# Optimization experiments

Hardware: AMD Instinct MI355X
Metric: run time of the kernel (lower is better)

The kernel has to match this reference:

```python
import jax, jax.numpy as jnp
import numpy as np

B, C, L = 8192, 1, 4096
SCALES = 5
OUT_DIM = 512
STD_FACTOR = 1.0
SQRT_HALF = 0.7071067811865476  # Haar filter coefficient 1/sqrt(2)


def setup_inputs() -> dict:
    key = jax.random.key(0)
    k1, k2 = jax.random.split(key)
    x = jax.random.normal(k1, (B, C, L), dtype=jnp.float32)
    # kaiming_uniform_(a=0): bound = sqrt(2) * sqrt(3 / fan_in)
    fan_in = L  # in_dim_wave == in_dim for dyadic Haar
    bound = np.sqrt(2.0) * np.sqrt(3.0 / fan_in)
    block_mat = jax.random.uniform(k2, (L, OUT_DIM), dtype=jnp.float32,
                                   minval=-bound, maxval=bound)
    return {"x": x, "block_mat": block_mat}


def haar_analysis(x, scales):
    """Multi-level Haar DWT over last axis. Returns [cA_n, cD_n, ..., cD_1]."""
    details = []
    cur = x
    for _ in range(scales):
        even, odd = cur[..., ::2], cur[..., 1::2]
        details.append((even - odd) * SQRT_HALF)  # highpass
        cur = (even + odd) * SQRT_HALF            # lowpass
    return [cur] + details[::-1]


def reference(x, block_mat):
    coeffs = haar_analysis(x, SCALES)
    x_freq_cat = jnp.concatenate(coeffs, axis=-1)        # [B, C, L]
    c_no = x_freq_cat.shape[-1]
    x_freq_mat = x_freq_cat.reshape(-1, c_no)            # [B*C, L]
    a = jnp.abs(x_freq_mat)
    # torch.std is unbiased (ddof=1)
    threshold = jnp.mean(a) + jnp.std(a, ddof=1) * STD_FACTOR
    mask = a > threshold
    # sparse.mm(sparse(masked x), W) == (x * mask) @ W
    x_sparse = jnp.where(mask, x_freq_mat, jnp.zeros((), x_freq_mat.dtype))
    out = jax.nn.relu(x_sparse @ block_mat)              # [B*C, OUT_DIM]
    return out.reshape(x_freq_cat.shape[:-1] + (OUT_DIM,))
```

## Files before the change

### kernel.cpp

```cpp
#include <hip/hip_runtime.h>
#include <hip/hip_bf16.h>
#include <math.h>

#define LDIM 4096
#define NROWS 8192
#define NOUT 512

static const float SQRT_HALF_F = 0.70710678118654752440f;

typedef __attribute__((ext_vector_type(8))) short short8;
typedef __attribute__((ext_vector_type(4))) float f32x4;
typedef __attribute__((ext_vector_type(8))) unsigned short u16x8;
typedef __attribute__((ext_vector_type(4))) unsigned short u16x4;
typedef __attribute__((ext_vector_type(2))) unsigned short u16x2;

#define AM_OFF   0ull
#define WT_OFF   67108864ull
#define PART_OFF (WT_OFF + 4194304ull)
#define THR_OFF  (PART_OFF + 131072ull)

__device__ inline unsigned short f2bf(float f) {
  union { float f; unsigned u; } v; v.f = f;
  unsigned r = (v.u + 0x7fffu + ((v.u >> 16) & 1u)) >> 16;
  return (unsigned short)r;
}

__device__ inline unsigned short mcvt(float f, float thr) {
  return f2bf((fabsf(f) > thr) ? f : 0.0f);
}

__device__ inline void async16(void* l, const void* g) {
  __builtin_amdgcn_global_load_lds((const __attribute__((address_space(1))) void*)g,
                                   (__attribute__((address_space(3))) void*)l, 16, 0, 0);
}


__global__ __launch_bounds__(256) void haar1_kernel(const float* __restrict__ x,
                                                    double* __restrict__ partials) {
  __shared__ double red[8];
  const int row = blockIdx.x;
  const int t = threadIdx.x;
  const float S = SQRT_HALF_F;

  const float4* xr = (const float4*)(x + (size_t)row * LDIM) + 4 * t;
  float v[16];
#pragma unroll
  for (int k = 0; k < 4; ++k) {
    float4 q = xr[k];
    v[4 * k] = q.x; v[4 * k + 1] = q.y; v[4 * k + 2] = q.z; v[4 * k + 3] = q.w;
  }

  double sa = 0.0, sq = 0.0;
  float a1[8], a2[4], a3[2], a4;
#pragma unroll
  for (int j = 0; j < 8; ++j) {
    float d = (v[2 * j] - v[2 * j + 1]) * S;
    a1[j] = (v[2 * j] + v[2 * j + 1]) * S;
    sa += (double)fabsf(d); sq += (double)d * (double)d;
  }
#pragma unroll
  for (int j = 0; j < 4; ++j) {
    float d = (a1[2 * j] - a1[2 * j + 1]) * S;
    a2[j] = (a1[2 * j] + a1[2 * j + 1]) * S;
    sa += (double)fabsf(d); sq += (double)d * (double)d;
  }
#pragma unroll
  for (int j = 0; j < 2; ++j) {
    float d = (a2[2 * j] - a2[2 * j + 1]) * S;
    a3[j] = (a2[2 * j] + a2[2 * j + 1]) * S;
    sa += (double)fabsf(d); sq += (double)d * (double)d;
  }
  {
    float d = (a3[0] - a3[1]) * S;
    a4 = (a3[0] + a3[1]) * S;
    sa += (double)fabsf(d); sq += (double)d * (double)d;
  }
  {
    float other = __shfl_xor(a4, 1, 64);
    if ((t & 1) == 0) {
      float d = (a4 - other) * S, ap = (a4 + other) * S;
      sa += (double)fabsf(d) + (double)fabsf(ap);
      sq += (double)d * (double)d + (double)ap * (double)ap;
    }
  }

  const int lane = t & 63, wid = t >> 6;
#pragma unroll
  for (int off = 32; off > 0; off >>= 1) {
    sa += __shfl_down(sa, off, 64);
    sq += __shfl_down(sq, off, 64);
  }
  if (lane == 0) { red[wid] = sa; red[4 + wid] = sq; }
  __syncthreads();
  if (t == 0) {
    partials[2 * (size_t)row + 0] = red[0] + red[1] + red[2] + red[3];
    partials[2 * (size_t)row + 1] = red[4] + red[5] + red[6] + red[7];
  }
}

__global__ __launch_bounds__(256) void thr_kernel(const double* __restrict__ partials,
                                                  float* __restrict__ thr) {
  __shared__ double red[8];
  const int tid = threadIdx.x;
  double sa = 0.0, sq = 0.0;
#pragma unroll
  for (int k = 0; k < NROWS / 256; ++k) {
    int i = tid + k * 256;
    sa += partials[2 * i + 0];
    sq += partials[2 * i + 1];
  }
  const int lane = tid & 63, wid = tid >> 6;
#pragma unroll
  for (int off = 32; off > 0; off >>= 1) {
    sa += __shfl_down(sa, off, 64);
    sq += __shfl_down(sq, off, 64);
  }
  if (lane == 0) { red[wid] = sa; red[4 + wid] = sq; }
  __syncthreads();
  if (tid == 0) {
    double s = red[0] + red[1] + red[2] + red[3];
    double q = red[4] + red[5] + red[6] + red[7];
    const double n = (double)NROWS * (double)LDIM;
    double mean = s / n;
    double var = (q - s * s / n) / (n - 1.0);
    *thr = (float)(mean + sqrt(var));
  }
}

__global__ __launch_bounds__(256) void haar2_kernel(const float* __restrict__ x,
                                                    const float* __restrict__ thrp,
                                                    unsigned short* __restrict__ Am) {
  const float thr = *thrp;
  const int row = blockIdx.x;
  const int t = threadIdx.x;
  const float S = SQRT_HALF_F;

  const float4* xr = (const float4*)(x + (size_t)row * LDIM) + 4 * t;
  float v[16];
#pragma unroll
  for (int k = 0; k < 4; ++k) {
    float4 q = xr[k];
    v[4 * k] = q.x; v[4 * k + 1] = q.y; v[4 * k + 2] = q.z; v[4 * k + 3] = q.w;
  }

  unsigned short* orow = Am + (size_t)row * LDIM;
  float a1[8], a2[4], a3[2], a4;

  u16x8 d1;
#pragma unroll
  for (int j = 0; j < 8; ++j) {
    float d = (v[2 * j] - v[2 * j + 1]) * S;
    a1[j] = (v[2 * j] + v[2 * j + 1]) * S;
    d1[j] = mcvt(d, thr);
  }
  *(u16x8*)(orow + 2048 + 8 * t) = d1;

  u16x4 d2;
#pragma unroll
  for (int j = 0; j < 4; ++j) {
    float d = (a1[2 * j] - a1[2 * j + 1]) * S;
    a2[j] = (a1[2 * j] + a1[2 * j + 1]) * S;
    d2[j] = mcvt(d, thr);
  }
  *(u16x4*)(orow + 1024 + 4 * t) = d2;

  u16x2 d3;
#pragma unroll
  for (int j = 0; j < 2; ++j) {
    float d = (a2[2 * j] - a2[2 * j + 1]) * S;
    a3[j] = (a2[2 * j] + a2[2 * j + 1]) * S;
    d3[j] = mcvt(d, thr);
  }
  *(u16x2*)(orow + 512 + 2 * t) = d3;

  {
    float d = (a3[0] - a3[1]) * S;
    a4 = (a3[0] + a3[1]) * S;
    orow[256 + t] = mcvt(d, thr);
  }
  {
    float other = __shfl_xor(a4, 1, 64);
    if ((t & 1) == 0) {
      float d = (a4 - other) * S, ap = (a4 + other) * S;
      orow[128 + t / 2] = mcvt(d, thr);
      orow[t / 2] = mcvt(ap, thr);
    }
  }
}

__global__ __launch_bounds__(256) void wcvt_kernel(const float* __restrict__ W,
                                                   unsigned short* __restrict__ Wt) {
  __shared__ float tile[32][33];
  const int bx = blockIdx.x;
  const int by = blockIdx.y;
  const int tx = threadIdx.x & 31, ty = threadIdx.x >> 5;
#pragma unroll
  for (int j = 0; j < 4; ++j)
    tile[ty + j * 8][tx] = W[(size_t)(by * 32 + ty + j * 8) * NOUT + bx * 32 + tx];
  __syncthreads();
#pragma unroll
  for (int j = 0; j < 4; ++j)
    Wt[(size_t)(bx * 32 + ty + j * 8) * LDIM + by * 32 + tx] = f2bf(tile[tx][ty + j * 8]);
}

__global__ __launch_bounds__(256) void gemm_kernel(const unsigned short* __restrict__ Am,
                                                   const unsigned short* __restrict__ Wt,
                                                   float* __restrict__ out) {
  __shared__ __align__(16) unsigned short As[128 * 64];
  __shared__ __align__(16) unsigned short Bs[64 * 64];

  const int tid = threadIdx.x;
  const int lane = tid & 63, w = tid >> 6;
  const int quad = lane >> 4, l15 = lane & 15;

  const int id = blockIdx.x;
  const int xcd = id & 7, slot = id >> 3;
  const int nblk = slot & 7;
  const int mblk = (slot >> 3) * 8 + xcd;
  const int n0 = nblk * 64, m0 = mblk * 128;

  f32x4 acc[2][4] = {};

  const int rl = lane >> 3;
  const int cg = (lane & 7) ^ rl;
  const unsigned short* AgBase = Am + (size_t)(m0 + rl) * LDIM + cg * 8;
  const unsigned short* BgBase = Wt + (size_t)(n0 + rl) * LDIM + cg * 8;

  for (int k0 = 0; k0 < LDIM; k0 += 64) {
#pragma unroll
    for (int j = 0; j < 4; ++j)
      async16(&As[(w * 4 + j) * 512], AgBase + (size_t)((w * 4 + j) * 8) * LDIM + k0);
#pragma unroll
    for (int j = 0; j < 2; ++j)
      async16(&Bs[(w * 2 + j) * 512], BgBase + (size_t)((w * 2 + j) * 8) * LDIM + k0);
    __syncthreads();

    short8 af[2][2], bf[4][2];
#pragma unroll
    for (int mi = 0; mi < 2; ++mi) {
      const int row = w * 32 + mi * 16 + l15;
#pragma unroll
      for (int ks = 0; ks < 2; ++ks)
        af[mi][ks] = *(const short8*)&As[row * 64 + ((ks * 4 + quad) ^ (row & 7)) * 8];
    }
#pragma unroll
    for (int ni = 0; ni < 4; ++ni) {
      const int row = ni * 16 + l15;
#pragma unroll
      for (int ks = 0; ks < 2; ++ks)
        bf[ni][ks] = *(const short8*)&Bs[row * 64 + ((ks * 4 + quad) ^ (row & 7)) * 8];
    }
#pragma unroll
    for (int ks = 0; ks < 2; ++ks)
#pragma unroll
      for (int mi = 0; mi < 2; ++mi)
#pragma unroll
        for (int ni = 0; ni < 4; ++ni)
          acc[mi][ni] = __builtin_amdgcn_mfma_f32_16x16x32_bf16(af[mi][ks], bf[ni][ks],
                                                                acc[mi][ni], 0, 0, 0);
    __syncthreads();
  }

#pragma unroll
  for (int mi = 0; mi < 2; ++mi) {
#pragma unroll
    for (int ni = 0; ni < 4; ++ni) {
      const int r0 = m0 + w * 32 + mi * 16 + quad * 4;
      const int c = n0 + ni * 16 + l15;
#pragma unroll
      for (int r = 0; r < 4; ++r)
        out[(size_t)(r0 + r) * NOUT + c] = fmaxf(acc[mi][ni][r], 0.0f);
    }
  }
}

extern "C" void kernel_launch(void* const* d_in, const int* in_sizes, int n_in,
                              void* d_out, int out_size, void* d_ws, size_t ws_size,
                              hipStream_t stream) {
  const float* x = (const float*)d_in[0];
  const float* W = (const float*)d_in[1];
  float* out = (float*)d_out;

  char* ws = (char*)d_ws;
  unsigned short* Am = (unsigned short*)(ws + AM_OFF);
  unsigned short* Wt = (unsigned short*)(ws + WT_OFF);
  double* partials = (double*)(ws + PART_OFF);
  float* thr = (float*)(ws + THR_OFF);

  haar1_kernel<<<NROWS, 256, 0, stream>>>(x, partials);
  wcvt_kernel<<<dim3(NOUT / 32, LDIM / 32), 256, 0, stream>>>(W, Wt);
  thr_kernel<<<1, 256, 0, stream>>>(partials, thr);
  haar2_kernel<<<NROWS, 256, 0, stream>>>(x, thr, Am);
  gemm_kernel<<<512, 256, 0, stream>>>(Am, Wt, out);
}
```

Before: 273.9 us.

## Fuse weight conversion into haar1, widen threshold reduction and GEMM block to 8 waves

The weight transpose-and-convert kernel is merged into haar1 as extra blocks, removing one launch and letting it overlap with the row statistics work. The threshold reduction now uses 1024 threads. The GEMM block grows to 512 threads arranged as a 4x2 wave grid, so each wave computes a 32x32 sub-tile instead of 32x64, aiming for more waves to hide latency. This lowers per-wave MFMA work and register use but cuts fragment reuse, and the haar1 path with a 32x33 float shared tile may change its occupancy.

```diff
diff --git a/kernel.cpp b/kernel.cpp
--- a/kernel.cpp
+++ b/kernel.cpp
@@ -34,9 +34,26 @@
                                    (__attribute__((address_space(3))) void*)l, 16, 0, 0);
 }
 
-
 __global__ __launch_bounds__(256) void haar1_kernel(const float* __restrict__ x,
-                                                    double* __restrict__ partials) {
+                                                    double* __restrict__ partials,
+                                                    const float* __restrict__ W,
+                                                    unsigned short* __restrict__ Wt) {
+  if (blockIdx.x >= NROWS) {
+    __shared__ float tile[32][33];
+    const int wb = blockIdx.x - NROWS;
+    const int bx = wb & 15;
+    const int by = wb >> 4;
+    const int tx = threadIdx.x & 31, ty = threadIdx.x >> 5;
+#pragma unroll
+    for (int j = 0; j < 4; ++j)
+      tile[ty + j * 8][tx] = W[(size_t)(by * 32 + ty + j * 8) * NOUT + bx * 32 + tx];
+    __syncthreads();
+#pragma unroll
+    for (int j = 0; j < 4; ++j)
+      Wt[(size_t)(bx * 32 + ty + j * 8) * LDIM + by * 32 + tx] = f2bf(tile[tx][ty + j * 8]);
+    return;
+  }
+
   __shared__ double red[8];
   const int row = blockIdx.x;
   const int t = threadIdx.x;
@@ -98,14 +115,14 @@
   }
 }
 
-__global__ __launch_bounds__(256) void thr_kernel(const double* __restrict__ partials,
-                                                  float* __restrict__ thr) {
-  __shared__ double red[8];
+__global__ __launch_bounds__(1024) void thr_kernel(const double* __restrict__ partials,
+                                                   float* __restrict__ thr) {
+  __shared__ double red[32];
   const int tid = threadIdx.x;
   double sa = 0.0, sq = 0.0;
 #pragma unroll
-  for (int k = 0; k < NROWS / 256; ++k) {
-    int i = tid + k * 256;
+  for (int k = 0; k < NROWS / 1024; ++k) {
+    int i = tid + k * 1024;
     sa += partials[2 * i + 0];
     sq += partials[2 * i + 1];
   }
@@ -115,11 +132,12 @@
     sa += __shfl_down(sa, off, 64);
     sq += __shfl_down(sq, off, 64);
   }
-  if (lane == 0) { red[wid] = sa; red[4 + wid] = sq; }
+  if (lane == 0) { red[wid] = sa; red[16 + wid] = sq; }
   __syncthreads();
   if (tid == 0) {
-    double s = red[0] + red[1] + red[2] + red[3];
-    double q = red[4] + red[5] + red[6] + red[7];
+    double s = 0.0, q = 0.0;
+#pragma unroll
+    for (int i = 0; i < 16; ++i) { s += red[i]; q += red[16 + i]; }
     const double n = (double)NROWS * (double)LDIM;
     double mean = s / n;
     double var = (q - s * s / n) / (n - 1.0);
@@ -188,22 +206,7 @@
   }
 }
 
-__global__ __launch_bounds__(256) void wcvt_kernel(const float* __restrict__ W,
-                                                   unsigned short* __restrict__ Wt) {
-  __shared__ float tile[32][33];
-  const int bx = blockIdx.x;
-  const int by = blockIdx.y;
-  const int tx = threadIdx.x & 31, ty = threadIdx.x >> 5;
-#pragma unroll
-  for (int j = 0; j < 4; ++j)
-    tile[ty + j * 8][tx] = W[(size_t)(by * 32 + ty + j * 8) * NOUT + bx * 32 + tx];
-  __syncthreads();
-#pragma unroll
-  for (int j = 0; j < 4; ++j)
-    Wt[(size_t)(bx * 32 + ty + j * 8) * LDIM + by * 32 + tx] = f2bf(tile[tx][ty + j * 8]);
-}
-
-__global__ __launch_bounds__(256) void gemm_kernel(const unsigned short* __restrict__ Am,
+__global__ __launch_bounds__(512) void gemm_kernel(const unsigned short* __restrict__ Am,
                                                    const unsigned short* __restrict__ Wt,
                                                    float* __restrict__ out) {
   __shared__ __align__(16) unsigned short As[128 * 64];
@@ -212,6 +215,7 @@
   const int tid = threadIdx.x;
   const int lane = tid & 63, w = tid >> 6;
   const int quad = lane >> 4, l15 = lane & 15;
+  const int wm = w >> 1, wn = w & 1;
 
   const int id = blockIdx.x;
   const int xcd = id & 7, slot = id >> 3;
@@ -219,7 +223,7 @@
   const int mblk = (slot >> 3) * 8 + xcd;
   const int n0 = nblk * 64, m0 = mblk * 128;
 
-  f32x4 acc[2][4] = {};
+  f32x4 acc[2][2] = {};
 
   const int rl = lane >> 3;
   const int cg = (lane & 7) ^ rl;
@@ -228,24 +232,22 @@
 
   for (int k0 = 0; k0 < LDIM; k0 += 64) {
 #pragma unroll
-    for (int j = 0; j < 4; ++j)
-      async16(&As[(w * 4 + j) * 512], AgBase + (size_t)((w * 4 + j) * 8) * LDIM + k0);
-#pragma unroll
     for (int j = 0; j < 2; ++j)
-      async16(&Bs[(w * 2 + j) * 512], BgBase + (size_t)((w * 2 + j) * 8) * LDIM + k0);
+      async16(&As[(w * 2 + j) * 512], AgBase + (size_t)((w * 2 + j) * 8) * LDIM + k0);
+    async16(&Bs[w * 512], BgBase + (size_t)(w * 8) * LDIM + k0);
     __syncthreads();
 
-    short8 af[2][2], bf[4][2];
+    short8 af[2][2], bf[2][2];
 #pragma unroll
     for (int mi = 0; mi < 2; ++mi) {
-      const int row = w * 32 + mi * 16 + l15;
+      const int row = wm * 32 + mi * 16 + l15;
 #pragma unroll
       for (int ks = 0; ks < 2; ++ks)
         af[mi][ks] = *(const short8*)&As[row * 64 + ((ks * 4 + quad) ^ (row & 7)) * 8];
     }
 #pragma unroll
-    for (int ni = 0; ni < 4; ++ni) {
-      const int row = ni * 16 + l15;
+    for (int ni = 0; ni < 2; ++ni) {
+      const int row = wn * 32 + ni * 16 + l15;
 #pragma unroll
       for (int ks = 0; ks < 2; ++ks)
         bf[ni][ks] = *(const short8*)&Bs[row * 64 + ((ks * 4 + quad) ^ (row & 7)) * 8];
@@ -255,7 +257,7 @@
 #pragma unroll
       for (int mi = 0; mi < 2; ++mi)
 #pragma unroll
-        for (int ni = 0; ni < 4; ++ni)
+        for (int ni = 0; ni < 2; ++ni)
           acc[mi][ni] = __builtin_amdgcn_mfma_f32_16x16x32_bf16(af[mi][ks], bf[ni][ks],
                                                                 acc[mi][ni], 0, 0, 0);
     __syncthreads();
@@ -264,9 +266,9 @@
 #pragma unroll
   for (int mi = 0; mi < 2; ++mi) {
 #pragma unroll
-    for (int ni = 0; ni < 4; ++ni) {
-      const int r0 = m0 + w * 32 + mi * 16 + quad * 4;
-      const int c = n0 + ni * 16 + l15;
+    for (int ni = 0; ni < 2; ++ni) {
+      const int r0 = m0 + wm * 32 + mi * 16 + quad * 4;
+      const int c = n0 + wn * 32 + ni * 16 + l15;
 #pragma unroll
       for (int r = 0; r < 4; ++r)
         out[(size_t)(r0 + r) * NOUT + c] = fmaxf(acc[mi][ni][r], 0.0f);
@@ -287,9 +289,8 @@
   double* partials = (double*)(ws + PART_OFF);
   float* thr = (float*)(ws + THR_OFF);
 
-  haar1_kernel<<<NROWS, 256, 0, stream>>>(x, partials);
-  wcvt_kernel<<<dim3(NOUT / 32, LDIM / 32), 256, 0, stream>>>(W, Wt);
-  thr_kernel<<<1, 256, 0, stream>>>(partials, thr);
+  haar1_kernel<<<NROWS + 2048, 256, 0, stream>>>(x, partials, W, Wt);
+  thr_kernel<<<1, 1024, 0, stream>>>(partials, thr);
   haar2_kernel<<<NROWS, 256, 0, stream>>>(x, thr, Am);
-  gemm_kernel<<<512, 256, 0, stream>>>(Am, Wt, out);
-}
+  gemm_kernel<<<512, 512, 0, stream>>>(Am, Wt, out);
+}
```

New measurement: 268.0 us. -2.2%, faster.
